# Kernel tuning notes

Hardware: AMD Instinct MI355X
Metric: run time of the kernel (lower is better)

The kernel has to match this reference:

```python
import jax, jax.numpy as jnp
import numpy as np

B, N, H = 4, 256, 128
T = 8  # triplet hidden width


def _linear_init(key, fan_in, fan_out):
    s = 1.0 / np.sqrt(fan_in)
    kw, kb = jax.random.split(key)
    W = jax.random.uniform(kw, (fan_in, fan_out), minval=-s, maxval=s, dtype=jnp.float32)
    b = jax.random.uniform(kb, (fan_out,), minval=-s, maxval=s, dtype=jnp.float32)
    return W, b


def setup_inputs() -> dict:
    key = jax.random.key(0)
    ks = jax.random.split(key, 16)
    inp = {
        "node_embeddings": jax.random.normal(ks[0], (B, N, H), dtype=jnp.float32),
        "edge_embeddings": jax.random.normal(ks[1], (B, N, H), dtype=jnp.float32),
        "graph_embeddings": jax.random.normal(ks[2], (B, H), dtype=jnp.float32),
        "previous_hidden": jax.random.normal(ks[3], (B, N, H), dtype=jnp.float32),
    }
    # message MLP: (z_i 2H, z_j 2H, edge_j H, graph H) = 6H -> H -> H -> H
    inp["Wm1"], inp["bm1"] = _linear_init(ks[4], 6 * H, H)
    inp["Wm2"], inp["bm2"] = _linear_init(ks[5], H, H)
    inp["Wm3"], inp["bm3"] = _linear_init(ks[6], H, H)
    # gate MLP: (z 2H, m H, edge H, graph H) = 5H -> H -> H (sigmoid)
    inp["Wg1"], inp["bg1"] = _linear_init(ks[7], 5 * H, H)
    inp["Wg2"], inp["bg2"] = _linear_init(ks[8], H, H)
    # readout: (z 2H, m H) = 3H -> H
    inp["Wr"], inp["br"] = _linear_init(ks[9], 3 * H, H)
    # triplet MLP: (node_j H, node_k H, node H, edge 3H, graph H) = 7H -> 8 (relu)
    inp["Wt1"], inp["bt1"] = _linear_init(ks[10], 7 * H, T)
    # triplet edge readout: 8 -> H
    inp["Wt2"], inp["bt2"] = _linear_init(ks[11], T, H)
    # layer norm params
    inp["gamma"] = jnp.ones((H,), dtype=jnp.float32)
    inp["beta"] = jnp.zeros((H,), dtype=jnp.float32)
    return inp


def reference(node_embeddings, edge_embeddings, graph_embeddings, previous_hidden,
              Wm1, bm1, Wm2, bm2, Wm3, bm3,
              Wg1, bg1, Wg2, bg2, Wr, br,
              Wt1, bt1, Wt2, bt2, gamma, beta):
    h = node_embeddings.shape[-1]
    z = jnp.concatenate([node_embeddings, previous_hidden], axis=-1)  # [B,N,2H]

    # ---- pairwise messages: decompose first linear so the 6H-wide concat is never built ----
    W_zi, W_zj = Wm1[: 2 * h], Wm1[2 * h: 4 * h]
    W_e, W_g = Wm1[4 * h: 5 * h], Wm1[5 * h:]
    u = z @ W_zi + (graph_embeddings @ W_g)[:, None, :] + bm1   # per-i part [B,N,H]
    v = z @ W_zj + edge_embeddings @ W_e                        # per-j part [B,N,H]
    h1 = jax.nn.relu(u[:, :, None, :] + v[:, None, :, :])       # [B,Ni,Nj,H]
    h2 = jax.nn.relu(h1 @ Wm2 + bm2)
    msgs = h2 @ Wm3 + bm3                                       # [B,Ni,Nj,H]
    m = jnp.max(msgs, axis=2)                                   # max over j -> [B,N,H]

    gb = jnp.broadcast_to(graph_embeddings[:, None, :], node_embeddings.shape)
    gate_in = jnp.concatenate([z, m, edge_embeddings, gb], axis=-1)  # [B,N,5H]
    g = jax.nn.sigmoid(jax.nn.relu(gate_in @ Wg1 + bg1) @ Wg2 + bg2)
    h_i = jnp.concatenate([z, m], axis=-1) @ Wr + br
    h_g = g * h_i + (1.0 - g) * previous_hidden

    # ---- triplet messages ----
    # pre-activation is separable over (j, k, i), so max over the N^2 (k,j) pairs
    # equals per-channel max_j + max_k (relu is monotone, max commutes with it).
    Wt_j, Wt_k, Wt_n = Wt1[:h], Wt1[h: 2 * h], Wt1[2 * h: 3 * h]
    Wt_e = Wt1[3 * h: 4 * h] + Wt1[4 * h: 5 * h] + Wt1[5 * h: 6 * h]
    Wt_g = Wt1[6 * h:]
    a_j = node_embeddings @ Wt_j   # [B,N,8]
    a_k = node_embeddings @ Wt_k   # [B,N,8]
    c = node_embeddings @ Wt_n + edge_embeddings @ Wt_e + (graph_embeddings @ Wt_g)[:, None, :] + bt1
    t_max = jax.nn.relu(c + jnp.max(a_j, axis=1, keepdims=True) + jnp.max(a_k, axis=1, keepdims=True))
    h_ij = t_max @ Wt2 + bt2       # [B,N,H]

    # ---- layer norm on gated hidden ----
    mu = jnp.mean(h_g, axis=-1, keepdims=True)
    var = jnp.mean(jnp.square(h_g - mu), axis=-1, keepdims=True)
    h_norm = (h_g - mu) * jax.lax.rsqrt(var + 1e-5) * gamma + beta
    return (h_norm, h_ij)
```

## Files before the change

kernel.cpp:

```cpp
#include <hip/hip_runtime.h>
#include <hip/hip_bf16.h>

typedef unsigned short u16;
typedef unsigned int u32;
typedef float f32x4 __attribute__((ext_vector_type(4)));
typedef float f32x16 __attribute__((ext_vector_type(16)));
typedef short s16x8 __attribute__((ext_vector_type(8)));

#define MFMA32(a,b,c) __builtin_amdgcn_mfma_f32_32x32x16_bf16((a),(b),(c),0,0,0)
#define MFMA16(a,b,c) __builtin_amdgcn_mfma_f32_16x16x32_bf16((a),(b),(c),0,0,0)

static __device__ __forceinline__ u16 f2bf(float x){
  union { __hip_bfloat16 b; u16 u; } c;
  c.b = __float2bfloat16(x);
  return c.u;
}
static __device__ __forceinline__ u32 pk2(float a, float b){
  return (u32)f2bf(a) | ((u32)f2bf(b) << 16);
}

static __device__ __forceinline__ void softbar() {
  __builtin_amdgcn_sched_barrier(0);
  asm volatile("s_waitcnt lgkmcnt(0)" ::: "memory");
  __builtin_amdgcn_s_barrier();
  __builtin_amdgcn_sched_barrier(0);
}

__global__ void prep_kernel(const float* __restrict__ Wm1, const float* __restrict__ Wm2,
                            const float* __restrict__ Wm3, const float* __restrict__ Wg1,
                            const float* __restrict__ Wr,  const float* __restrict__ Wt1,
                            const float* __restrict__ Wg2,
                            const float* __restrict__ node,const float* __restrict__ prev,
                            const float* __restrict__ edge,const float* __restrict__ graph,
                            u16* __restrict__ WbT, u16* __restrict__ WgrT,
                            u16* __restrict__ Wm2T, u16* __restrict__ Wm3T,
                            u16* __restrict__ Wg2T, u16* __restrict__ gin)
{
  int idx = blockIdx.x * 256 + threadIdx.x;
  if (idx < 147456) {
    int n = idx >> 9, k = idx & 511;
    int part = k >> 7, kk = k & 127;
    float v = 0.f;
    if (n < 128) {
      if (part == 0)      v = Wm1[kk*128 + n];
      else if (part == 1) v = Wm1[(128+kk)*128 + n];
      else if (part == 3) v = Wm1[(640+kk)*128 + n];
    } else if (n < 256) {
      int nn = n - 128;
      if (part == 0)      v = Wm1[(256+kk)*128 + nn];
      else if (part == 1) v = Wm1[(384+kk)*128 + nn];
      else if (part == 2) v = Wm1[(512+kk)*128 + nn];
    } else if (n < 280) {
      int tt = n - 256;
      if (tt < 8)       { if (part == 0) v = Wt1[kk*8 + tt]; }
      else if (tt < 16) { if (part == 0) v = Wt1[(128+kk)*8 + (tt-8)]; }
      else {
        int t = tt - 16;
        if (part == 0)      v = Wt1[(256+kk)*8 + t];
        else if (part == 2) v = Wt1[(384+kk)*8 + t] + Wt1[(512+kk)*8 + t] + Wt1[(640+kk)*8 + t];
        else if (part == 3) v = Wt1[(768+kk)*8 + t];
      }
    }
    WbT[idx] = f2bf(v);
    return;
  }
  idx -= 147456;
  if (idx < 163840) {
    int n = idx / 640, k = idx - n*640;
    int part = k >> 7, kk = k & 127;
    float v = 0.f;
    if (n < 128) {
      int r = (part==0) ? kk : (part==1) ? (128+kk) : (part==2) ? (384+kk)
                        : (part==3) ? (512+kk) : (256+kk);
      v = Wg1[r*128 + n];
    } else {
      int nn = n - 128;
      if (part == 0)      v = Wr[kk*128 + nn];
      else if (part == 1) v = Wr[(128+kk)*128 + nn];
      else if (part == 4) v = Wr[(256+kk)*128 + nn];
    }
    WgrT[idx] = f2bf(v);
    return;
  }
  idx -= 163840;
  if (idx < 16384) { int n = idx >> 7, k = idx & 127; Wm2T[idx] = f2bf(Wm2[k*128 + n]); return; }
  idx -= 16384;
  if (idx < 16384) { int n = idx >> 7, k = idx & 127; Wm3T[idx] = f2bf(Wm3[k*128 + n]); return; }
  idx -= 16384;
  if (idx < 16384) { int n = idx >> 7, k = idx & 127; Wg2T[idx] = f2bf(Wg2[k*128 + n]); return; }
  idx -= 16384;
  {
    int row = idx >> 9, k = idx & 511;
    int part = k >> 7, kk = k & 127;
    float v;
    if (part == 0)      v = node[row*128 + kk];
    else if (part == 1) v = prev[row*128 + kk];
    else if (part == 2) v = edge[row*128 + kk];
    else                v = graph[(row >> 8)*128 + kk];
    gin[row*640 + k] = f2bf(v);
  }
}

__global__ __launch_bounds__(256) void gemm_uvt_kernel(const u16* __restrict__ gin,
                                                       const u16* __restrict__ WbT,
                                                       float* __restrict__ uvt)
{
  int m0 = blockIdx.x * 16, n0 = blockIdx.y * 16;
  int tid = threadIdx.x;
  int w = tid >> 6, lane = tid & 63;
  int c = lane & 15, g = lane >> 4;
  __shared__ float cpart[4][16][17];
  const u16* arow = gin + (size_t)(m0 + c) * 640;
  const u16* brow = WbT + (size_t)(n0 + c) * 512;
  f32x4 acc = {0.f, 0.f, 0.f, 0.f};
#pragma unroll
  for (int kk = 0; kk < 4; ++kk) {
    int k0 = w*4 + kk;
    s16x8 a = *reinterpret_cast<const s16x8*>(arow + k0*32 + g*8);
    s16x8 b = *reinterpret_cast<const s16x8*>(brow + k0*32 + g*8);
    acc = MFMA16(a, b, acc);
  }
#pragma unroll
  for (int r = 0; r < 4; ++r) cpart[w][g*4 + r][c] = acc[r];
  __syncthreads();
  int row = tid >> 4, col = tid & 15;
  float s = cpart[0][row][col] + cpart[1][row][col]
          + cpart[2][row][col] + cpart[3][row][col];
  uvt[(size_t)(m0 + row) * 288 + n0 + col] = s;
}

__global__ __launch_bounds__(256) void msgmax_kernel(const float* __restrict__ uvt,
    const u16* __restrict__ Wm2T, const u16* __restrict__ Wm3T,
    const float* __restrict__ bm1, const float* __restrict__ bm2,
    const float* __restrict__ bm3, u16* __restrict__ gin, float* __restrict__ mjk)
{
  const int bx   = blockIdx.x;
  const int row0 = bx * 2;
  const int b    = row0 >> 8;
  const int tid = threadIdx.x;
  const int w   = tid >> 6;
  const int lane = tid & 63;
  const int jc = lane & 31;
  const int hi = lane >> 5;
  const int colbase = w * 32;

  __shared__ u16 a1s[2][32][136];
  __shared__ u16 h2s[2][32][136];
  __shared__ float part[4][16];

  s16x8 wb2[8], wb3[8];
#pragma unroll
  for (int ks = 0; ks < 8; ++ks) {
    wb2[ks] = *reinterpret_cast<const s16x8*>(Wm2T + (colbase + jc)*128 + ks*16 + hi*8);
    wb3[ks] = *reinterpret_cast<const s16x8*>(Wm3T + (colbase + jc)*128 + ks*16 + hi*8);
  }

  const int bj = lane >> 3;
  const int bk = (lane & 7) * 16;
  f32x4 uf[2][4];
#pragma unroll
  for (int i = 0; i < 2; ++i) {
    const float* urow = uvt + (size_t)(row0 + i) * 288;
#pragma unroll
    for (int q = 0; q < 4; ++q)
      uf[i][q] = *reinterpret_cast<const f32x4*>(urow + bk + q*4)
               + *reinterpret_cast<const f32x4*>(bm1 + bk + q*4);
  }
  f32x4 bm2v[4];
#pragma unroll
  for (int grp = 0; grp < 4; ++grp)
    bm2v[grp] = *reinterpret_cast<const f32x4*>(bm2 + colbase + grp*8 + 4*hi);

  const f32x4 z4 = {0.f, 0.f, 0.f, 0.f};
  float mm[2][16];
#pragma unroll
  for (int i = 0; i < 2; ++i)
#pragma unroll
    for (int t = 0; t < 16; ++t) mm[i][t] = -1e30f;

  const float* vb = uvt + (size_t)(b*256) * 288 + 128;
  f32x4 vc[4];
#define LOADV(IT) do { \
  const float* p_ = vb + (size_t)((IT)*32 + w*8 + bj) * 288 + bk; \
  vc[0] = *reinterpret_cast<const f32x4*>(p_); \
  vc[1] = *reinterpret_cast<const f32x4*>(p_ + 4); \
  vc[2] = *reinterpret_cast<const f32x4*>(p_ + 8); \
  vc[3] = *reinterpret_cast<const f32x4*>(p_ + 12); } while (0)

  LOADV(0);

  for (int it = 0; it < 8; ++it) {
#pragma unroll
    for (int i = 0; i < 2; ++i) {
#pragma unroll
      for (int q = 0; q < 2; ++q) {
        f32x4 lo = __builtin_elementwise_max(vc[2*q]   + uf[i][2*q],   z4);
        f32x4 hn = __builtin_elementwise_max(vc[2*q+1] + uf[i][2*q+1], z4);
        uint4 pk = {pk2(lo[0], lo[1]), pk2(lo[2], lo[3]),
                    pk2(hn[0], hn[1]), pk2(hn[2], hn[3])};
        *reinterpret_cast<uint4*>(&a1s[i][w*8 + bj][bk + q*8]) = pk;
      }
    }
    if (it < 7) LOADV(it + 1);
    softbar();

#pragma unroll
    for (int i = 0; i < 2; ++i) {
      f32x16 acc1;
#pragma unroll
      for (int grp = 0; grp < 4; ++grp)
#pragma unroll
        for (int r = 0; r < 4; ++r) acc1[grp*4 + r] = bm2v[grp][r];
#pragma unroll
      for (int ks = 0; ks < 8; ++ks) {
        s16x8 bf = *reinterpret_cast<const s16x8*>(&a1s[i][jc][ks*16 + hi*8]);
        acc1 = MFMA32(wb2[ks], bf, acc1);
      }
#pragma unroll
      for (int grp = 0; grp < 4; ++grp) {
        float v0 = fmaxf(acc1[grp*4+0], 0.f), v1 = fmaxf(acc1[grp*4+1], 0.f);
        float v2 = fmaxf(acc1[grp*4+2], 0.f), v3 = fmaxf(acc1[grp*4+3], 0.f);
        uint2 pk = {pk2(v0, v1), pk2(v2, v3)};
        *reinterpret_cast<uint2*>(&h2s[i][jc][colbase + grp*8 + 4*hi]) = pk;
      }
    }
    softbar();

#pragma unroll
    for (int i = 0; i < 2; ++i) {
      f32x16 acc2 = {0.f,0.f,0.f,0.f,0.f,0.f,0.f,0.f,
                     0.f,0.f,0.f,0.f,0.f,0.f,0.f,0.f};
#pragma unroll
      for (int ks = 0; ks < 8; ++ks) {
        s16x8 bf = *reinterpret_cast<const s16x8*>(&h2s[i][jc][ks*16 + hi*8]);
        acc2 = MFMA32(wb3[ks], bf, acc2);
      }
#pragma unroll
      for (int t = 0; t < 16; ++t) mm[i][t] = fmaxf(mm[i][t], acc2[t]);
    }
  }
#undef LOADV

#pragma unroll
  for (int i = 0; i < 2; ++i) {
#pragma unroll
    for (int t = 0; t < 16; ++t) {
      mm[i][t] = fmaxf(mm[i][t], __shfl_xor(mm[i][t], 1));
      mm[i][t] = fmaxf(mm[i][t], __shfl_xor(mm[i][t], 2));
      mm[i][t] = fmaxf(mm[i][t], __shfl_xor(mm[i][t], 4));
      mm[i][t] = fmaxf(mm[i][t], __shfl_xor(mm[i][t], 8));
      mm[i][t] = fmaxf(mm[i][t], __shfl_xor(mm[i][t], 16));
    }
    if (jc == 0) {
#pragma unroll
      for (int grp = 0; grp < 4; ++grp) {
        int col = colbase + grp*8 + 4*hi;
        uint2 pk = {pk2(mm[i][grp*4+0] + bm3[col],   mm[i][grp*4+1] + bm3[col+1]),
                    pk2(mm[i][grp*4+2] + bm3[col+2], mm[i][grp*4+3] + bm3[col+3])};
        *reinterpret_cast<uint2*>(gin + (size_t)(row0 + i)*640 + 512 + col) = pk;
      }
    }
  }

  if (bx < 4) {
    __syncthreads();
    int rr = bx*256 + tid;
    float v[16];
#pragma unroll
    for (int t = 0; t < 16; ++t) v[t] = uvt[(size_t)rr*288 + 256 + t];
#pragma unroll
    for (int off = 32; off >= 1; off >>= 1) {
#pragma unroll
      for (int t = 0; t < 16; ++t) v[t] = fmaxf(v[t], __shfl_xor(v[t], off));
    }
    int wid = tid >> 6;
    if ((tid & 63) == 0) {
#pragma unroll
      for (int t = 0; t < 16; ++t) part[wid][t] = v[t];
    }
    __syncthreads();
    if (tid < 16)
      mjk[bx*16 + tid] = fmaxf(fmaxf(part[0][tid], part[1][tid]),
                               fmaxf(part[2][tid], part[3][tid]));
  }
}

__global__ __launch_bounds__(256) void gate_finalize_kernel(
    const u16* __restrict__ gin, const u16* __restrict__ WgrT,
    const u16* __restrict__ Wg2T,
    const float* __restrict__ bg1, const float* __restrict__ br,
    const float* __restrict__ bg2, const float* __restrict__ prev,
    const float* __restrict__ uvt, const float* __restrict__ mjk,
    const float* __restrict__ bt1, const float* __restrict__ Wt2,
    const float* __restrict__ bt2, const float* __restrict__ gamma,
    const float* __restrict__ beta, float* __restrict__ out)
{
  const int m0 = blockIdx.x * 16;
  const int tid = threadIdx.x;
  const int w = tid >> 6, lane = tid & 63;
  const int c = lane & 15, g = lane >> 4;

  __shared__ u16 at[16][648];
  __shared__ u16 r1b[16][136];
  __shared__ float his[16][132];
  __shared__ float gls[16][132];

#pragma unroll
  for (int q = 0; q < 5; ++q) {
    int idx = q*256 + tid;
    int r = idx / 80, kk = (idx - r*80) * 8;
    *reinterpret_cast<uint4*>(&at[r][kk]) =
      *reinterpret_cast<const uint4*>(gin + (size_t)(m0 + r)*640 + kk);
  }
  __syncthreads();

#pragma unroll
  for (int nt = 0; nt < 4; ++nt) {
    int n0 = w*64 + nt*16;
    const u16* brow = WgrT + (size_t)(n0 + c) * 640;
    f32x4 acc = {0.f, 0.f, 0.f, 0.f};
#pragma unroll
    for (int k0 = 0; k0 < 20; ++k0) {
      s16x8 a = *reinterpret_cast<const s16x8*>(&at[c][k0*32 + g*8]);
      s16x8 b = *reinterpret_cast<const s16x8*>(brow + k0*32 + g*8);
      acc = MFMA16(a, b, acc);
    }
    int ocol = n0 + c;
#pragma unroll
    for (int r = 0; r < 4; ++r) {
      int orow = g*4 + r;
      if (ocol < 128) {
        float val = fmaxf(acc[r] + bg1[ocol], 0.f);
        r1b[orow][ocol] = f2bf(val);
      } else {
        his[orow][ocol - 128] = acc[r] + br[ocol - 128];
      }
    }
  }
  __syncthreads();

#pragma unroll
  for (int nt = 0; nt < 2; ++nt) {
    int n0 = w*32 + nt*16;
    const u16* brow = Wg2T + (size_t)(n0 + c) * 128;
    f32x4 acc = {0.f, 0.f, 0.f, 0.f};
#pragma unroll
    for (int k0 = 0; k0 < 4; ++k0) {
      s16x8 a = *reinterpret_cast<const s16x8*>(&r1b[c][k0*32 + g*8]);
      s16x8 b = *reinterpret_cast<const s16x8*>(brow + k0*32 + g*8);
      acc = MFMA16(a, b, acc);
    }
    int ocol = n0 + c;
#pragma unroll
    for (int r = 0; r < 4; ++r)
      gls[g*4 + r][ocol] = acc[r] + bg2[ocol];
  }
  __syncthreads();

  const int row = tid >> 4;
  const int cb = (tid & 15) * 8;
  const int grow = m0 + row;
  const int bb = grow >> 8;
  const float* prow = prev + (size_t)grow * 128 + cb;

  float hgv[8];
  float s1 = 0.f, s2 = 0.f;
#pragma unroll
  for (int q = 0; q < 8; ++q) {
    float gl = gls[row][cb + q];
    float gg = 1.f / (1.f + __expf(-gl));
    float hg = gg * his[row][cb + q] + (1.f - gg) * prow[q];
    hgv[q] = hg; s1 += hg; s2 += hg*hg;
  }
#pragma unroll
  for (int off = 1; off < 16; off <<= 1) {
    s1 += __shfl_xor(s1, off);
    s2 += __shfl_xor(s2, off);
  }
  float mu  = s1 * 0.0078125f;
  float var = s2 * 0.0078125f - mu*mu;
  float rs  = rsqrtf(var + 1e-5f);
#pragma unroll
  for (int q = 0; q < 8; ++q) {
    int col = cb + q;
    out[(size_t)grow*128 + col] = (hgv[q] - mu) * rs * gamma[col] + beta[col];
  }

  float tv[8];
  const float* crow = uvt + (size_t)grow * 288 + 272;
#pragma unroll
  for (int t = 0; t < 8; ++t)
    tv[t] = fmaxf(crow[t] + bt1[t] + mjk[bb*16 + t] + mjk[bb*16 + 8 + t], 0.f);
#pragma unroll
  for (int q = 0; q < 8; ++q) {
    int col = cb + q;
    float o2 = bt2[col];
#pragma unroll
    for (int t = 0; t < 8; ++t) o2 += tv[t] * Wt2[t*128 + col];
    out[131072 + (size_t)grow*128 + col] = o2;
  }
}

extern "C" void kernel_launch(void* const* d_in, const int* in_sizes, int n_in,
                              void* d_out, int out_size, void* d_ws, size_t ws_size,
                              hipStream_t stream) {
  const float* node  = (const float*)d_in[0];
  const float* edge  = (const float*)d_in[1];
  const float* graph = (const float*)d_in[2];
  const float* prev  = (const float*)d_in[3];
  const float* Wm1 = (const float*)d_in[4];
  const float* bm1 = (const float*)d_in[5];
  const float* Wm2 = (const float*)d_in[6];
  const float* bm2 = (const float*)d_in[7];
  const float* Wm3 = (const float*)d_in[8];
  const float* bm3 = (const float*)d_in[9];
  const float* Wg1 = (const float*)d_in[10];
  const float* bg1 = (const float*)d_in[11];
  const float* Wg2 = (const float*)d_in[12];
  const float* bg2 = (const float*)d_in[13];
  const float* Wr  = (const float*)d_in[14];
  const float* br  = (const float*)d_in[15];
  const float* Wt1 = (const float*)d_in[16];
  const float* bt1 = (const float*)d_in[17];
  const float* Wt2 = (const float*)d_in[18];
  const float* bt2 = (const float*)d_in[19];
  const float* gamma = (const float*)d_in[20];
  const float* beta  = (const float*)d_in[21];
  float* out = (float*)d_out;

  char* ws = (char*)d_ws;
  u16*   WbT  = (u16*)(ws + 0);
  u16*   WgrT = (u16*)(ws + 294912);
  u16*   Wm2T = (u16*)(ws + 622592);
  u16*   Wm3T = (u16*)(ws + 655360);
  u16*   gin  = (u16*)(ws + 688128);
  float* uvt  = (float*)(ws + 1998848);
  u16*   Wg2T = (u16*)(ws + 3178496);
  float* mjk  = (float*)(ws + 3211264);

  prep_kernel<<<3456, 256, 0, stream>>>(Wm1, Wm2, Wm3, Wg1, Wr, Wt1, Wg2,
                                        node, prev, edge, graph,
                                        WbT, WgrT, Wm2T, Wm3T, Wg2T, gin);
  gemm_uvt_kernel<<<dim3(64, 18), 256, 0, stream>>>(gin, WbT, uvt);
  msgmax_kernel<<<512, 256, 0, stream>>>(uvt, Wm2T, Wm3T, bm1, bm2, bm3, gin, mjk);
  gate_finalize_kernel<<<64, 256, 0, stream>>>(gin, WgrT, Wg2T, bg1, br, bg2,
                                               prev, uvt, mjk, bt1, Wt2, bt2,
                                               gamma, beta, out);
}
```

Baseline: 64.20 us.

## Drop bf16 activation staging buffer; convert fp32 inputs inside GEMM kernels

The prep kernel no longer packs node/prev/edge/graph into a bf16 concatenated 'gin' buffer. The uvt GEMM and the gate kernel now read the fp32 inputs directly and convert them to bf16 fragments in registers. The message output goes to a small separate buffer. The uvt GEMM is also retiled: each wave computes its own 16 rows over the full K instead of splitting K across waves with an LDS reduction. This removes a full write and read of the staging buffer plus the LDS reduction. In exchange the GEMMs do redundant fp32 loads and conversions and hold more registers for the A fragments.

```diff
diff --git a/kernel.cpp b/kernel.cpp
--- a/kernel.cpp
+++ b/kernel.cpp
@@ -18,6 +18,12 @@
 static __device__ __forceinline__ u32 pk2(float a, float b){
   return (u32)f2bf(a) | ((u32)f2bf(b) << 16);
 }
+static __device__ __forceinline__ s16x8 pk8(float4 x, float4 y){
+  s16x8 f;
+  f[0]=(short)f2bf(x.x); f[1]=(short)f2bf(x.y); f[2]=(short)f2bf(x.z); f[3]=(short)f2bf(x.w);
+  f[4]=(short)f2bf(y.x); f[5]=(short)f2bf(y.y); f[6]=(short)f2bf(y.z); f[7]=(short)f2bf(y.w);
+  return f;
+}
 
 static __device__ __forceinline__ void softbar() {
   __builtin_amdgcn_sched_barrier(0);
@@ -30,11 +36,9 @@
                             const float* __restrict__ Wm3, const float* __restrict__ Wg1,
                             const float* __restrict__ Wr,  const float* __restrict__ Wt1,
                             const float* __restrict__ Wg2,
-                            const float* __restrict__ node,const float* __restrict__ prev,
-                            const float* __restrict__ edge,const float* __restrict__ graph,
                             u16* __restrict__ WbT, u16* __restrict__ WgrT,
                             u16* __restrict__ Wm2T, u16* __restrict__ Wm3T,
-                            u16* __restrict__ Wg2T, u16* __restrict__ gin)
+                            u16* __restrict__ Wg2T)
 {
   int idx = blockIdx.x * 256 + threadIdx.x;
   if (idx < 147456) {
@@ -87,52 +91,53 @@
   idx -= 16384;
   if (idx < 16384) { int n = idx >> 7, k = idx & 127; Wm3T[idx] = f2bf(Wm3[k*128 + n]); return; }
   idx -= 16384;
-  if (idx < 16384) { int n = idx >> 7, k = idx & 127; Wg2T[idx] = f2bf(Wg2[k*128 + n]); return; }
-  idx -= 16384;
-  {
-    int row = idx >> 9, k = idx & 511;
-    int part = k >> 7, kk = k & 127;
-    float v;
-    if (part == 0)      v = node[row*128 + kk];
-    else if (part == 1) v = prev[row*128 + kk];
-    else if (part == 2) v = edge[row*128 + kk];
-    else                v = graph[(row >> 8)*128 + kk];
-    gin[row*640 + k] = f2bf(v);
-  }
-}
-
-__global__ __launch_bounds__(256) void gemm_uvt_kernel(const u16* __restrict__ gin,
-                                                       const u16* __restrict__ WbT,
-                                                       float* __restrict__ uvt)
+  { int n = idx >> 7, k = idx & 127; Wg2T[idx] = f2bf(Wg2[k*128 + n]); }
+}
+
+static __device__ __forceinline__ s16x8 src_frag(
+    const float* __restrict__ node, const float* __restrict__ prev,
+    const float* __restrict__ edge, const float* __restrict__ graph,
+    int row, int part, int kk)
 {
-  int m0 = blockIdx.x * 16, n0 = blockIdx.y * 16;
+  const float* s;
+  if      (part == 0) s = node  + (size_t)row * 128;
+  else if (part == 1) s = prev  + (size_t)row * 128;
+  else if (part == 2) s = edge  + (size_t)row * 128;
+  else                s = graph + (size_t)(row >> 8) * 128;
+  float4 x = *reinterpret_cast<const float4*>(s + kk);
+  float4 y = *reinterpret_cast<const float4*>(s + kk + 4);
+  return pk8(x, y);
+}
+
+__global__ __launch_bounds__(256) void gemm_uvt_kernel(
+    const float* __restrict__ node, const float* __restrict__ prev,
+    const float* __restrict__ edge, const float* __restrict__ graph,
+    const u16* __restrict__ WbT, float* __restrict__ uvt)
+{
+  int m0 = blockIdx.x * 64, n0 = blockIdx.y * 16;
   int tid = threadIdx.x;
   int w = tid >> 6, lane = tid & 63;
   int c = lane & 15, g = lane >> 4;
-  __shared__ float cpart[4][16][17];
-  const u16* arow = gin + (size_t)(m0 + c) * 640;
+  int row = m0 + w*16 + c;
   const u16* brow = WbT + (size_t)(n0 + c) * 512;
   f32x4 acc = {0.f, 0.f, 0.f, 0.f};
 #pragma unroll
-  for (int kk = 0; kk < 4; ++kk) {
-    int k0 = w*4 + kk;
-    s16x8 a = *reinterpret_cast<const s16x8*>(arow + k0*32 + g*8);
+  for (int k0 = 0; k0 < 16; ++k0) {
+    int part = k0 >> 2;
+    int kk = (k0 & 3)*32 + g*8;
+    s16x8 a = src_frag(node, prev, edge, graph, row, part, kk);
     s16x8 b = *reinterpret_cast<const s16x8*>(brow + k0*32 + g*8);
     acc = MFMA16(a, b, acc);
   }
 #pragma unroll
-  for (int r = 0; r < 4; ++r) cpart[w][g*4 + r][c] = acc[r];
-  __syncthreads();
-  int row = tid >> 4, col = tid & 15;
-  float s = cpart[0][row][col] + cpart[1][row][col]
-          + cpart[2][row][col] + cpart[3][row][col];
-  uvt[(size_t)(m0 + row) * 288 + n0 + col] = s;
+  for (int r = 0; r < 4; ++r)
+    uvt[(size_t)(m0 + w*16 + g*4 + r) * 288 + n0 + c] = acc[r];
 }
 
 __global__ __launch_bounds__(256) void msgmax_kernel(const float* __restrict__ uvt,
     const u16* __restrict__ Wm2T, const u16* __restrict__ Wm3T,
     const float* __restrict__ bm1, const float* __restrict__ bm2,
-    const float* __restrict__ bm3, u16* __restrict__ gin, float* __restrict__ mjk)
+    const float* __restrict__ bm3, u16* __restrict__ mbuf, float* __restrict__ mjk)
 {
   const int bx   = blockIdx.x;
   const int row0 = bx * 2;
@@ -257,7 +262,7 @@
         int col = colbase + grp*8 + 4*hi;
         uint2 pk = {pk2(mm[i][grp*4+0] + bm3[col],   mm[i][grp*4+1] + bm3[col+1]),
                     pk2(mm[i][grp*4+2] + bm3[col+2], mm[i][grp*4+3] + bm3[col+3])};
-        *reinterpret_cast<uint2*>(gin + (size_t)(row0 + i)*640 + 512 + col) = pk;
+        *reinterpret_cast<uint2*>(mbuf + (size_t)(row0 + i)*128 + col) = pk;
       }
     }
   }
@@ -286,10 +291,12 @@
 }
 
 __global__ __launch_bounds__(256) void gate_finalize_kernel(
-    const u16* __restrict__ gin, const u16* __restrict__ WgrT,
+    const float* __restrict__ node, const float* __restrict__ prev,
+    const float* __restrict__ edge, const float* __restrict__ graph,
+    const u16* __restrict__ mbuf, const u16* __restrict__ WgrT,
     const u16* __restrict__ Wg2T,
     const float* __restrict__ bg1, const float* __restrict__ br,
-    const float* __restrict__ bg2, const float* __restrict__ prev,
+    const float* __restrict__ bg2,
     const float* __restrict__ uvt, const float* __restrict__ mjk,
     const float* __restrict__ bt1, const float* __restrict__ Wt2,
     const float* __restrict__ bt2, const float* __restrict__ gamma,
@@ -300,19 +307,18 @@
   const int w = tid >> 6, lane = tid & 63;
   const int c = lane & 15, g = lane >> 4;
 
-  __shared__ u16 at[16][648];
   __shared__ u16 r1b[16][136];
   __shared__ float his[16][132];
   __shared__ float gls[16][132];
 
-#pragma unroll
-  for (int q = 0; q < 5; ++q) {
-    int idx = q*256 + tid;
-    int r = idx / 80, kk = (idx - r*80) * 8;
-    *reinterpret_cast<uint4*>(&at[r][kk]) =
-      *reinterpret_cast<const uint4*>(gin + (size_t)(m0 + r)*640 + kk);
-  }
-  __syncthreads();
+  const int arow = m0 + c;
+  s16x8 af[20];
+#pragma unroll
+  for (int k0 = 0; k0 < 16; ++k0)
+    af[k0] = src_frag(node, prev, edge, graph, arow, k0 >> 2, (k0 & 3)*32 + g*8);
+#pragma unroll
+  for (int k0 = 16; k0 < 20; ++k0)
+    af[k0] = *reinterpret_cast<const s16x8*>(mbuf + (size_t)arow*128 + (k0-16)*32 + g*8);
 
 #pragma unroll
   for (int nt = 0; nt < 4; ++nt) {
@@ -321,9 +327,8 @@
     f32x4 acc = {0.f, 0.f, 0.f, 0.f};
 #pragma unroll
     for (int k0 = 0; k0 < 20; ++k0) {
-      s16x8 a = *reinterpret_cast<const s16x8*>(&at[c][k0*32 + g*8]);
       s16x8 b = *reinterpret_cast<const s16x8*>(brow + k0*32 + g*8);
-      acc = MFMA16(a, b, acc);
+      acc = MFMA16(af[k0], b, acc);
     }
     int ocol = n0 + c;
 #pragma unroll
@@ -433,17 +438,18 @@
   u16*   WgrT = (u16*)(ws + 294912);
   u16*   Wm2T = (u16*)(ws + 622592);
   u16*   Wm3T = (u16*)(ws + 655360);
-  u16*   gin  = (u16*)(ws + 688128);
-  float* uvt  = (float*)(ws + 1998848);
-  u16*   Wg2T = (u16*)(ws + 3178496);
-  float* mjk  = (float*)(ws + 3211264);
-
-  prep_kernel<<<3456, 256, 0, stream>>>(Wm1, Wm2, Wm3, Wg1, Wr, Wt1, Wg2,
-                                        node, prev, edge, graph,
-                                        WbT, WgrT, Wm2T, Wm3T, Wg2T, gin);
-  gemm_uvt_kernel<<<dim3(64, 18), 256, 0, stream>>>(gin, WbT, uvt);
-  msgmax_kernel<<<512, 256, 0, stream>>>(uvt, Wm2T, Wm3T, bm1, bm2, bm3, gin, mjk);
-  gate_finalize_kernel<<<64, 256, 0, stream>>>(gin, WgrT, Wg2T, bg1, br, bg2,
-                                               prev, uvt, mjk, bt1, Wt2, bt2,
+  u16*   Wg2T = (u16*)(ws + 688128);
+  float* uvt  = (float*)(ws + 720896);
+  u16*   mbuf = (u16*)(ws + 1900544);
+  float* mjk  = (float*)(ws + 2162688);
+
+  prep_kernel<<<1408, 256, 0, stream>>>(Wm1, Wm2, Wm3, Wg1, Wr, Wt1, Wg2,
+                                        WbT, WgrT, Wm2T, Wm3T, Wg2T);
+  gemm_uvt_kernel<<<dim3(16, 18), 256, 0, stream>>>(node, prev, edge, graph,
+                                                    WbT, uvt);
+  msgmax_kernel<<<512, 256, 0, stream>>>(uvt, Wm2T, Wm3T, bm1, bm2, bm3, mbuf, mjk);
+  gate_finalize_kernel<<<64, 256, 0, stream>>>(node, prev, edge, graph, mbuf,
+                                               WgrT, Wg2T, bg1, br, bg2,
+                                               uvt, mjk, bt1, Wt2, bt2,
                                                gamma, beta, out);
 }
```

Measured after the change: 74.66 us. +16.3%, slower.
